# Kernel optimization log

Hardware: AMD Instinct MI355X
Metric: run time of the kernel (lower is better)

## Reference

```python
import jax, jax.numpy as jnp
import numpy as np

N_NODES = 50000
N_EDGES = 800000
DIM_IN = 64
DIM_HID = 128
DIM_OUT = 64


def _linear_init(key, fan_in, fan_out):
    # torch nn.Linear default: U(-1/sqrt(fan_in), 1/sqrt(fan_in)) for W and b
    kw, kb = jax.random.split(key)
    bound = 1.0 / np.sqrt(fan_in)
    W = jax.random.uniform(kw, (fan_in, fan_out), minval=-bound, maxval=bound, dtype=jnp.float32)
    b = jax.random.uniform(kb, (fan_out,), minval=-bound, maxval=bound, dtype=jnp.float32)
    return W, b


def setup_inputs() -> dict:
    key = jax.random.key(0)
    kx, ke, k0, k1, k2 = jax.random.split(key, 5)
    x = jax.random.normal(kx, (N_NODES, DIM_IN), dtype=jnp.float32)
    edge_idx = jax.random.randint(ke, (2, N_EDGES), 0, N_NODES, dtype=jnp.int64)
    W0, b0 = _linear_init(k0, 2 * DIM_IN, DIM_HID)
    W1, b1 = _linear_init(k1, DIM_HID, DIM_HID)
    W2, b2 = _linear_init(k2, DIM_HID, DIM_OUT)
    return {"x": x, "edge_idx": edge_idx, "W0": W0, "b0": b0,
            "W1": W1, "b1": b1, "W2": W2, "b2": b2}


def reference(x, edge_idx, W0, b0, W1, b1, W2, b2):
    row, col = edge_idx[0], edge_idx[1]
    # gather + concat edge features: [E, 2*dim_in]
    h = jnp.concatenate([x[row], x[col]], axis=-1)
    h = jax.nn.softplus(h @ W0 + b0)
    h = jax.nn.softplus(h @ W1 + b1)
    h = h @ W2 + b2  # [E, dim_out]
    # scatter-add edge messages to source nodes
    return jax.ops.segment_sum(h, row, num_segments=x.shape[0])
```

## Files before the change

### kernel.cpp

```cpp
#include <hip/hip_runtime.h>
#include <math.h>

#define N_NODES 50000
#define N_EDGES 800000
#define DIM_IN 64
#define DIM_HID 128
#define DIM_OUT 64
#define PAD 136

typedef __attribute__((ext_vector_type(8))) short short8;
typedef __attribute__((ext_vector_type(4))) float f32x4;

union U8 { uint4 u; short8 s; };

__device__ __forceinline__ unsigned short f2bf(float f) {
    unsigned u = __float_as_uint(f);
    return (unsigned short)((u + 0x7fffu + ((u >> 16) & 1u)) >> 16);
}

__device__ __forceinline__ unsigned cvt_pk_bf16(float a, float b) {
    unsigned d;
    asm("v_cvt_pk_bf16_f32 %0, %1, %2" : "=v"(d) : "v"(a), "v"(b));
    return d;
}

__device__ __forceinline__ float exp2_fast(float a) {
#if __has_builtin(__builtin_amdgcn_exp2f)
    return __builtin_amdgcn_exp2f(a);
#else
    return __expf(a * 0.69314718f);
#endif
}

__device__ __forceinline__ unsigned sp2(float x0, float x1) {
    const float L2E = 1.44269504f;
    float z0 = exp2_fast(-fabsf(x0) * L2E);
    float z1 = exp2_fast(-fabsf(x1) * L2E);
    float p0 = fmaf(fmaf(fmaf(-0.1011458f, z0, 0.2942925f), z0, -0.5f), z0, 1.0f) * z0;
    float p1 = fmaf(fmaf(fmaf(-0.1011458f, z1, 0.2942925f), z1, -0.5f), z1, 1.0f) * z1;
    return cvt_pk_bf16(fmaxf(x0, 0.0f) + p0, fmaxf(x1, 0.0f) + p1);
}

__global__ void prep_all(const float* __restrict__ x,
                         const float* __restrict__ W0,
                         const float* __restrict__ W1,
                         const float* __restrict__ W2,
                         unsigned short* __restrict__ wt,
                         unsigned short* __restrict__ xbf,
                         float4* __restrict__ outz) {
    int i = blockIdx.x * blockDim.x + threadIdx.x;

    if (i < (N_NODES * DIM_OUT / 4))
        outz[i] = make_float4(0.f, 0.f, 0.f, 0.f);

    if (i < (N_NODES * DIM_IN / 4)) {
        float4 v = *((const float4*)x + i);
        uint2 p;
        p.x = cvt_pk_bf16(v.x, v.y);
        p.y = cvt_pk_bf16(v.z, v.w);
        *((uint2*)xbf + i) = p;
    }

    if (i < 320 * PAD) {
        int row = i / PAD, s = i - row * PAD;
        float v = 0.f;
        if (s < 128) {
            int f = ((s >> 5) << 5) | (((s & 7) >> 2) << 4) | (((s >> 3) & 3) << 2) | (s & 3);
            if (row < 128)      v = W0[s * DIM_HID + row];
            else if (row < 256) v = W1[f * DIM_HID + (row - 128)];
            else                v = W2[f * DIM_OUT + (row - 256)];
        }
        wt[i] = f2bf(v);
    }
}

__global__ void prep_weights(const float* __restrict__ W0,
                             const float* __restrict__ W1,
                             const float* __restrict__ W2,
                             unsigned short* __restrict__ wt) {
    int i = blockIdx.x * blockDim.x + threadIdx.x;
    if (i >= 320 * PAD) return;
    int row = i / PAD, s = i - row * PAD;
    float v = 0.f;
    if (s < 128) {
        int f = ((s >> 5) << 5) | (((s & 7) >> 2) << 4) | (((s >> 3) & 3) << 2) | (s & 3);
        if (row < 128)      v = W0[s * DIM_HID + row];
        else if (row < 256) v = W1[f * DIM_HID + (row - 128)];
        else                v = W2[f * DIM_OUT + (row - 256)];
    }
    wt[i] = f2bf(v);
}

template <bool XB>
__global__ __launch_bounds__(256, 4)
void edge_mlp_mfma(const float* __restrict__ x,
                   const unsigned short* __restrict__ xbf,
                   const int* __restrict__ eidx,
                   const unsigned short* __restrict__ wt,
                   const float* __restrict__ b0,
                   const float* __restrict__ b1,
                   const float* __restrict__ b2,
                   float* __restrict__ out) {
    const int lane = threadIdx.x & 63;
    const int w    = threadIdx.x >> 6;
    const int l16  = lane & 15;
    const int q    = lane >> 4;
    const int e0w  = blockIdx.x * 128 + w * 32;

    const unsigned short* Wt0 = wt;
    const unsigned short* Wt1 = wt + 128 * PAD;
    const unsigned short* Wt2 = wt + 256 * PAD;

    int nodeR[2], nodeC[2];
#pragma unroll
    for (int m = 0; m < 2; ++m) {
        nodeR[m] = eidx[e0w + m * 16 + l16];
        nodeC[m] = eidx[N_EDGES + e0w + m * 16 + l16];
    }

    short8 hfr[2][4];
#pragma unroll
    for (int m = 0; m < 2; ++m)
#pragma unroll
        for (int kk = 0; kk < 4; ++kk) {
            int node = (kk >= 2) ? nodeC[m] : nodeR[m];
            if (XB) {
                hfr[m][kk] = *(const short8*)(xbf + (size_t)node * DIM_IN + (kk & 1) * 32 + q * 8);
            } else {
                const float* p = x + (size_t)node * DIM_IN + (kk & 1) * 32 + q * 8;
                float4 v0 = *(const float4*)p;
                float4 v1 = *(const float4*)(p + 4);
                U8 t;
                t.u.x = cvt_pk_bf16(v0.x, v0.y);
                t.u.y = cvt_pk_bf16(v0.z, v0.w);
                t.u.z = cvt_pk_bf16(v1.x, v1.y);
                t.u.w = cvt_pk_bf16(v1.z, v1.w);
                hfr[m][kk] = t.s;
            }
        }

#pragma unroll
    for (int L = 0; L < 2; ++L) {
        const unsigned short* W = L ? Wt1 : Wt0;
        const float* bias = L ? b1 : b0;
        unsigned d[2][8][2];
#pragma unroll
        for (int ti = 0; ti < 8; ++ti) {
            f32x4 bb = *(const f32x4*)(bias + ti * 16 + q * 4);
            f32x4 a0 = bb, a1 = bb;
            const unsigned short* Wp = W + (ti * 16 + l16) * PAD + q * 8;
            short8 wf[4];
#pragma unroll
            for (int kk = 0; kk < 4; ++kk)
                wf[kk] = *(const short8*)(Wp + kk * 32);
#pragma unroll
            for (int kk = 0; kk < 4; ++kk) {
                a0 = __builtin_amdgcn_mfma_f32_16x16x32_bf16(wf[kk], hfr[0][kk], a0, 0, 0, 0);
                a1 = __builtin_amdgcn_mfma_f32_16x16x32_bf16(wf[kk], hfr[1][kk], a1, 0, 0, 0);
            }
            d[0][ti][0] = sp2(a0[0], a0[1]);
            d[0][ti][1] = sp2(a0[2], a0[3]);
            d[1][ti][0] = sp2(a1[0], a1[1]);
            d[1][ti][1] = sp2(a1[2], a1[3]);
        }
#pragma unroll
        for (int m = 0; m < 2; ++m)
#pragma unroll
            for (int kk = 0; kk < 4; ++kk) {
                U8 t;
                t.u.x = d[m][2 * kk][0];
                t.u.y = d[m][2 * kk][1];
                t.u.z = d[m][2 * kk + 1][0];
                t.u.w = d[m][2 * kk + 1][1];
                hfr[m][kk] = t.s;
            }
    }

    int nodeO[2][4];
#pragma unroll
    for (int m = 0; m < 2; ++m)
#pragma unroll
        for (int r = 0; r < 4; ++r)
            nodeO[m][r] = eidx[e0w + m * 16 + q * 4 + r];

#pragma unroll
    for (int ti = 0; ti < 4; ++ti) {
        float bv = b2[ti * 16 + l16];
        f32x4 a0 = (f32x4){bv, bv, bv, bv};
        f32x4 a1 = a0;
        const unsigned short* Wp = Wt2 + (ti * 16 + l16) * PAD + q * 8;
        short8 wf[4];
#pragma unroll
        for (int kk = 0; kk < 4; ++kk)
            wf[kk] = *(const short8*)(Wp + kk * 32);
#pragma unroll
        for (int kk = 0; kk < 4; ++kk) {
            a0 = __builtin_amdgcn_mfma_f32_16x16x32_bf16(hfr[0][kk], wf[kk], a0, 0, 0, 0);
            a1 = __builtin_amdgcn_mfma_f32_16x16x32_bf16(hfr[1][kk], wf[kk], a1, 0, 0, 0);
        }
#pragma unroll
        for (int r = 0; r < 4; ++r) {
            atomicAdd(out + (size_t)nodeO[0][r] * DIM_OUT + ti * 16 + l16, a0[r]);
            atomicAdd(out + (size_t)nodeO[1][r] * DIM_OUT + ti * 16 + l16, a1[r]);
        }
    }
}

extern "C" void kernel_launch(void* const* d_in, const int* in_sizes, int n_in,
                              void* d_out, int out_size, void* d_ws, size_t ws_size,
                              hipStream_t stream) {
    const float* x  = (const float*)d_in[0];
    const int*   ei = (const int*)d_in[1];
    const float* W0 = (const float*)d_in[2];
    const float* b0 = (const float*)d_in[3];
    const float* W1 = (const float*)d_in[4];
    const float* b1 = (const float*)d_in[5];
    const float* W2 = (const float*)d_in[6];
    const float* b2 = (const float*)d_in[7];
    float* out = (float*)d_out;

    unsigned short* wt = (unsigned short*)d_ws;
    const size_t WT_BYTES = (size_t)320 * PAD * sizeof(unsigned short);
    unsigned short* xbf = (unsigned short*)((char*)d_ws + WT_BYTES);
    const size_t need = WT_BYTES + (size_t)N_NODES * DIM_IN * sizeof(unsigned short);

    if (ws_size >= need) {
        prep_all<<<(N_NODES * DIM_IN / 4 + 255) / 256, 256, 0, stream>>>(
            x, W0, W1, W2, wt, xbf, (float4*)out);
        edge_mlp_mfma<true><<<N_EDGES / 128, 256, 0, stream>>>(
            x, xbf, ei, wt, b0, b1, b2, out);
    } else {
        hipMemsetAsync(out, 0, (size_t)N_NODES * DIM_OUT * sizeof(float), stream);
        const int wn = 320 * PAD;
        prep_weights<<<(wn + 255) / 256, 256, 0, stream>>>(W0, W1, W2, wt);
        edge_mlp_mfma<false><<<N_EDGES / 128, 256, 0, stream>>>(
            x, nullptr, ei, wt, b0, b1, b2, out);
    }
}
```

Measured before the change: 274.8 us.

## Counting-sort edges by source node and pre-reduce messages before atomics

Adds a counting sort of edges by row: a histogram kernel, a single-block scan and an atomic scatter that writes sorted row and column arrays. The MLP kernel then reads edges in sorted order. Each lane sums the consecutive outputs that share a destination node before issuing float atomics, cutting atomic traffic and contention and improving gather locality. The cost is three extra launches plus the scatter atomics. The fallback path now passes wt as the xbf pointer to prep_all, so the x conversion can overwrite the packed weights there.

```diff
diff --git a/kernel.cpp b/kernel.cpp
--- a/kernel.cpp
+++ b/kernel.cpp
@@ -47,7 +47,8 @@
                          const float* __restrict__ W2,
                          unsigned short* __restrict__ wt,
                          unsigned short* __restrict__ xbf,
-                         float4* __restrict__ outz) {
+                         float4* __restrict__ outz,
+                         int* __restrict__ hist) {
     int i = blockIdx.x * blockDim.x + threadIdx.x;
 
     if (i < (N_NODES * DIM_OUT / 4))
@@ -60,6 +61,8 @@
         p.y = cvt_pk_bf16(v.z, v.w);
         *((uint2*)xbf + i) = p;
     }
+
+    if (hist && i < N_NODES) hist[i] = 0;
 
     if (i < 320 * PAD) {
         int row = i / PAD, s = i - row * PAD;
@@ -74,27 +77,56 @@
     }
 }
 
-__global__ void prep_weights(const float* __restrict__ W0,
-                             const float* __restrict__ W1,
-                             const float* __restrict__ W2,
-                             unsigned short* __restrict__ wt) {
+__global__ void hist_kernel(const int* __restrict__ eidx, int* __restrict__ hist) {
     int i = blockIdx.x * blockDim.x + threadIdx.x;
-    if (i >= 320 * PAD) return;
-    int row = i / PAD, s = i - row * PAD;
-    float v = 0.f;
-    if (s < 128) {
-        int f = ((s >> 5) << 5) | (((s & 7) >> 2) << 4) | (((s >> 3) & 3) << 2) | (s & 3);
-        if (row < 128)      v = W0[s * DIM_HID + row];
-        else if (row < 256) v = W1[f * DIM_HID + (row - 128)];
-        else                v = W2[f * DIM_OUT + (row - 256)];
-    }
-    wt[i] = f2bf(v);
-}
-
-template <bool XB>
+    if (i < N_EDGES) atomicAdd(&hist[eidx[i]], 1);
+}
+
+__global__ __launch_bounds__(1024)
+void scan_bins(const int* __restrict__ hist, int* __restrict__ cursor) {
+    __shared__ int part[1024];
+    const int t = threadIdx.x;
+    const int CH = (N_NODES + 1023) / 1024;
+    const int base = t * CH;
+    int s = 0;
+    for (int j = 0; j < CH; ++j) {
+        int b = base + j;
+        if (b < N_NODES) s += hist[b];
+    }
+    part[t] = s;
+    __syncthreads();
+    for (int off = 1; off < 1024; off <<= 1) {
+        int u = (t >= off) ? part[t - off] : 0;
+        __syncthreads();
+        part[t] += u;
+        __syncthreads();
+    }
+    int run = (t == 0) ? 0 : part[t - 1];
+    for (int j = 0; j < CH; ++j) {
+        int b = base + j;
+        if (b < N_NODES) { cursor[b] = run; run += hist[b]; }
+    }
+}
+
+__global__ void scatter_kernel(const int* __restrict__ eidx,
+                               int* __restrict__ cursor,
+                               int* __restrict__ srow,
+                               int* __restrict__ scol) {
+    int i = blockIdx.x * blockDim.x + threadIdx.x;
+    if (i >= N_EDGES) return;
+    int r = eidx[i];
+    int c = eidx[N_EDGES + i];
+    int pos = atomicAdd(&cursor[r], 1);
+    srow[pos] = r;
+    scol[pos] = c;
+}
+
+template <int MODE>
 __global__ __launch_bounds__(256, 4)
 void edge_mlp_mfma(const float* __restrict__ x,
                    const unsigned short* __restrict__ xbf,
+                   const int* __restrict__ srow,
+                   const int* __restrict__ scol,
                    const int* __restrict__ eidx,
                    const unsigned short* __restrict__ wt,
                    const float* __restrict__ b0,
@@ -114,9 +146,22 @@
     int nodeR[2], nodeC[2];
 #pragma unroll
     for (int m = 0; m < 2; ++m) {
-        nodeR[m] = eidx[e0w + m * 16 + l16];
-        nodeC[m] = eidx[N_EDGES + e0w + m * 16 + l16];
-    }
+        if (MODE == 2) {
+            nodeR[m] = srow[e0w + m * 16 + l16];
+            nodeC[m] = scol[e0w + m * 16 + l16];
+        } else {
+            nodeR[m] = eidx[e0w + m * 16 + l16];
+            nodeC[m] = eidx[N_EDGES + e0w + m * 16 + l16];
+        }
+    }
+
+    int ns[8];
+#pragma unroll
+    for (int m = 0; m < 2; ++m)
+#pragma unroll
+        for (int r = 0; r < 4; ++r)
+            ns[m * 4 + r] = (MODE == 2) ? srow[e0w + m * 16 + q * 4 + r]
+                                        : eidx[e0w + m * 16 + q * 4 + r];
 
     short8 hfr[2][4];
 #pragma unroll
@@ -124,7 +169,7 @@
 #pragma unroll
         for (int kk = 0; kk < 4; ++kk) {
             int node = (kk >= 2) ? nodeC[m] : nodeR[m];
-            if (XB) {
+            if (MODE >= 1) {
                 hfr[m][kk] = *(const short8*)(xbf + (size_t)node * DIM_IN + (kk & 1) * 32 + q * 8);
             } else {
                 const float* p = x + (size_t)node * DIM_IN + (kk & 1) * 32 + q * 8;
@@ -176,32 +221,60 @@
             }
     }
 
-    int nodeO[2][4];
-#pragma unroll
-    for (int m = 0; m < 2; ++m)
-#pragma unroll
-        for (int r = 0; r < 4; ++r)
-            nodeO[m][r] = eidx[e0w + m * 16 + q * 4 + r];
-
-#pragma unroll
-    for (int ti = 0; ti < 4; ++ti) {
-        float bv = b2[ti * 16 + l16];
-        f32x4 a0 = (f32x4){bv, bv, bv, bv};
-        f32x4 a1 = a0;
-        const unsigned short* Wp = Wt2 + (ti * 16 + l16) * PAD + q * 8;
-        short8 wf[4];
-#pragma unroll
-        for (int kk = 0; kk < 4; ++kk)
-            wf[kk] = *(const short8*)(Wp + kk * 32);
-#pragma unroll
-        for (int kk = 0; kk < 4; ++kk) {
-            a0 = __builtin_amdgcn_mfma_f32_16x16x32_bf16(hfr[0][kk], wf[kk], a0, 0, 0, 0);
-            a1 = __builtin_amdgcn_mfma_f32_16x16x32_bf16(hfr[1][kk], wf[kk], a1, 0, 0, 0);
-        }
-#pragma unroll
-        for (int r = 0; r < 4; ++r) {
-            atomicAdd(out + (size_t)nodeO[0][r] * DIM_OUT + ti * 16 + l16, a0[r]);
-            atomicAdd(out + (size_t)nodeO[1][r] * DIM_OUT + ti * 16 + l16, a1[r]);
+    {
+        f32x4 acc[4][2];
+#pragma unroll
+        for (int ti = 0; ti < 4; ++ti) {
+            float bv = b2[ti * 16 + l16];
+            f32x4 a0 = (f32x4){bv, bv, bv, bv};
+            f32x4 a1 = a0;
+            const unsigned short* Wp = Wt2 + (ti * 16 + l16) * PAD + q * 8;
+            short8 wf[4];
+#pragma unroll
+            for (int kk = 0; kk < 4; ++kk)
+                wf[kk] = *(const short8*)(Wp + kk * 32);
+#pragma unroll
+            for (int kk = 0; kk < 4; ++kk) {
+                a0 = __builtin_amdgcn_mfma_f32_16x16x32_bf16(hfr[0][kk], wf[kk], a0, 0, 0, 0);
+                a1 = __builtin_amdgcn_mfma_f32_16x16x32_bf16(hfr[1][kk], wf[kk], a1, 0, 0, 0);
+            }
+            acc[ti][0] = a0;
+            acc[ti][1] = a1;
+        }
+
+        if (MODE == 2) {
+            int curn = ns[0];
+            float c0 = 0.f, c1 = 0.f, c2 = 0.f, c3 = 0.f;
+#pragma unroll
+            for (int s = 0; s < 8; ++s) {
+                const int m = s >> 2, r = s & 3;
+                if (s > 0 && ns[s] != curn) {
+                    float* o = out + (size_t)curn * DIM_OUT + l16;
+                    atomicAdd(o +  0, c0);
+                    atomicAdd(o + 16, c1);
+                    atomicAdd(o + 32, c2);
+                    atomicAdd(o + 48, c3);
+                    c0 = c1 = c2 = c3 = 0.f;
+                    curn = ns[s];
+                }
+                c0 += acc[0][m][r];
+                c1 += acc[1][m][r];
+                c2 += acc[2][m][r];
+                c3 += acc[3][m][r];
+            }
+            float* o = out + (size_t)curn * DIM_OUT + l16;
+            atomicAdd(o +  0, c0);
+            atomicAdd(o + 16, c1);
+            atomicAdd(o + 32, c2);
+            atomicAdd(o + 48, c3);
+        } else {
+#pragma unroll
+            for (int ti = 0; ti < 4; ++ti)
+#pragma unroll
+                for (int r = 0; r < 4; ++r) {
+                    atomicAdd(out + (size_t)ns[r] * DIM_OUT + ti * 16 + l16, acc[ti][0][r]);
+                    atomicAdd(out + (size_t)ns[4 + r] * DIM_OUT + ti * 16 + l16, acc[ti][1][r]);
+                }
         }
     }
 }
@@ -219,21 +292,40 @@
     const float* b2 = (const float*)d_in[7];
     float* out = (float*)d_out;
 
-    unsigned short* wt = (unsigned short*)d_ws;
-    const size_t WT_BYTES = (size_t)320 * PAD * sizeof(unsigned short);
-    unsigned short* xbf = (unsigned short*)((char*)d_ws + WT_BYTES);
-    const size_t need = WT_BYTES + (size_t)N_NODES * DIM_IN * sizeof(unsigned short);
-
-    if (ws_size >= need) {
+    char* ws = (char*)d_ws;
+    const size_t WT_BYTES   = (size_t)320 * PAD * 2;
+    const size_t XBF_BYTES  = (size_t)N_NODES * DIM_IN * 2;
+    const size_t HIST_BYTES = 200192;
+    const size_t SROW_BYTES = (size_t)N_EDGES * 4;
+
+    unsigned short* wt  = (unsigned short*)ws;
+    unsigned short* xbf = (unsigned short*)(ws + WT_BYTES);
+    int* hist   = (int*)(ws + WT_BYTES + XBF_BYTES);
+    int* cursor = (int*)(ws + WT_BYTES + XBF_BYTES + HIST_BYTES);
+    int* srow   = (int*)(ws + WT_BYTES + XBF_BYTES + 2 * HIST_BYTES);
+    int* scol   = (int*)(ws + WT_BYTES + XBF_BYTES + 2 * HIST_BYTES + SROW_BYTES);
+
+    const size_t need_sorted = WT_BYTES + XBF_BYTES + 2 * HIST_BYTES + 2 * SROW_BYTES;
+    const size_t need_xbf    = WT_BYTES + XBF_BYTES;
+
+    if (ws_size >= need_sorted) {
         prep_all<<<(N_NODES * DIM_IN / 4 + 255) / 256, 256, 0, stream>>>(
-            x, W0, W1, W2, wt, xbf, (float4*)out);
-        edge_mlp_mfma<true><<<N_EDGES / 128, 256, 0, stream>>>(
-            x, xbf, ei, wt, b0, b1, b2, out);
+            x, W0, W1, W2, wt, xbf, (float4*)out, hist);
+        hist_kernel<<<(N_EDGES + 255) / 256, 256, 0, stream>>>(ei, hist);
+        scan_bins<<<1, 1024, 0, stream>>>(hist, cursor);
+        scatter_kernel<<<(N_EDGES + 255) / 256, 256, 0, stream>>>(ei, cursor, srow, scol);
+        edge_mlp_mfma<2><<<N_EDGES / 128, 256, 0, stream>>>(
+            x, xbf, srow, scol, ei, wt, b0, b1, b2, out);
+    } else if (ws_size >= need_xbf) {
+        prep_all<<<(N_NODES * DIM_IN / 4 + 255) / 256, 256, 0, stream>>>(
+            x, W0, W1, W2, wt, xbf, (float4*)out, nullptr);
+        edge_mlp_mfma<1><<<N_EDGES / 128, 256, 0, stream>>>(
+            x, xbf, nullptr, nullptr, ei, wt, b0, b1, b2, out);
     } else {
         hipMemsetAsync(out, 0, (size_t)N_NODES * DIM_OUT * sizeof(float), stream);
-        const int wn = 320 * PAD;
-        prep_weights<<<(wn + 255) / 256, 256, 0, stream>>>(W0, W1, W2, wt);
-        edge_mlp_mfma<false><<<N_EDGES / 128, 256, 0, stream>>>(
-            x, nullptr, ei, wt, b0, b1, b2, out);
-    }
-}
+        prep_all<<<(N_NODES * DIM_IN / 4 + 255) / 256, 256, 0, stream>>>(
+            x, W0, W1, W2, wt, (unsigned short*)wt, (float4*)out, nullptr);
+        edge_mlp_mfma<0><<<N_EDGES / 128, 256, 0, stream>>>(
+            x, nullptr, nullptr, nullptr, ei, wt, b0, b1, b2, out);
+    }
+}
```

Result: slower. 448.6 us (+63.3%).

## Stage layer weights in LDS per block instead of global loads

Applied to the files above, without the earlier changes.

Each block copies the bf16 weight matrix for the current layer into a 34 KB shared buffer and reads MFMA operand fragments from LDS rather than global/L2. The buffer is reloaded between layers, with barriers around each copy, and the destination-node index loads are moved earlier. The final-layer results are gathered into registers before the atomic scatter. This trades repeated global weight reads for per-block copy traffic, extra syncs and LDS that may limit occupancy.

```diff
diff --git a/kernel.cpp b/kernel.cpp
--- a/kernel.cpp
+++ b/kernel.cpp
@@ -101,22 +101,27 @@
                    const float* __restrict__ b1,
                    const float* __restrict__ b2,
                    float* __restrict__ out) {
+    __shared__ unsigned short lw[128 * PAD];
+
     const int lane = threadIdx.x & 63;
     const int w    = threadIdx.x >> 6;
     const int l16  = lane & 15;
     const int q    = lane >> 4;
     const int e0w  = blockIdx.x * 128 + w * 32;
 
-    const unsigned short* Wt0 = wt;
-    const unsigned short* Wt1 = wt + 128 * PAD;
-    const unsigned short* Wt2 = wt + 256 * PAD;
-
     int nodeR[2], nodeC[2];
 #pragma unroll
     for (int m = 0; m < 2; ++m) {
         nodeR[m] = eidx[e0w + m * 16 + l16];
         nodeC[m] = eidx[N_EDGES + e0w + m * 16 + l16];
     }
+
+    int ns[8];
+#pragma unroll
+    for (int m = 0; m < 2; ++m)
+#pragma unroll
+        for (int r = 0; r < 4; ++r)
+            ns[m * 4 + r] = eidx[e0w + m * 16 + q * 4 + r];
 
     short8 hfr[2][4];
 #pragma unroll
@@ -139,16 +144,22 @@
             }
         }
 
+    {
+        const uint4* src = (const uint4*)wt;
+        uint4* dst = (uint4*)lw;
+        for (int i = threadIdx.x; i < 2176; i += 256) dst[i] = src[i];
+    }
+    __syncthreads();
+
 #pragma unroll
     for (int L = 0; L < 2; ++L) {
-        const unsigned short* W = L ? Wt1 : Wt0;
         const float* bias = L ? b1 : b0;
         unsigned d[2][8][2];
 #pragma unroll
         for (int ti = 0; ti < 8; ++ti) {
             f32x4 bb = *(const f32x4*)(bias + ti * 16 + q * 4);
             f32x4 a0 = bb, a1 = bb;
-            const unsigned short* Wp = W + (ti * 16 + l16) * PAD + q * 8;
+            const unsigned short* Wp = lw + (ti * 16 + l16) * PAD + q * 8;
             short8 wf[4];
 #pragma unroll
             for (int kk = 0; kk < 4; ++kk)
@@ -174,35 +185,44 @@
                 t.u.w = d[m][2 * kk + 1][1];
                 hfr[m][kk] = t.s;
             }
-    }
-
-    int nodeO[2][4];
-#pragma unroll
-    for (int m = 0; m < 2; ++m)
-#pragma unroll
-        for (int r = 0; r < 4; ++r)
-            nodeO[m][r] = eidx[e0w + m * 16 + q * 4 + r];
-
-#pragma unroll
-    for (int ti = 0; ti < 4; ++ti) {
-        float bv = b2[ti * 16 + l16];
-        f32x4 a0 = (f32x4){bv, bv, bv, bv};
-        f32x4 a1 = a0;
-        const unsigned short* Wp = Wt2 + (ti * 16 + l16) * PAD + q * 8;
-        short8 wf[4];
-#pragma unroll
-        for (int kk = 0; kk < 4; ++kk)
-            wf[kk] = *(const short8*)(Wp + kk * 32);
-#pragma unroll
-        for (int kk = 0; kk < 4; ++kk) {
-            a0 = __builtin_amdgcn_mfma_f32_16x16x32_bf16(hfr[0][kk], wf[kk], a0, 0, 0, 0);
-            a1 = __builtin_amdgcn_mfma_f32_16x16x32_bf16(hfr[1][kk], wf[kk], a1, 0, 0, 0);
-        }
-#pragma unroll
-        for (int r = 0; r < 4; ++r) {
-            atomicAdd(out + (size_t)nodeO[0][r] * DIM_OUT + ti * 16 + l16, a0[r]);
-            atomicAdd(out + (size_t)nodeO[1][r] * DIM_OUT + ti * 16 + l16, a1[r]);
-        }
+        __syncthreads();
+        {
+            const uint4* src = (const uint4*)(wt + (size_t)(L ? 256 : 128) * PAD);
+            uint4* dst = (uint4*)lw;
+            const int n = L ? 1088 : 2176;
+            for (int i = threadIdx.x; i < n; i += 256) dst[i] = src[i];
+        }
+        __syncthreads();
+    }
+
+    {
+        f32x4 acc[4][2];
+#pragma unroll
+        for (int ti = 0; ti < 4; ++ti) {
+            float bv = b2[ti * 16 + l16];
+            f32x4 a0 = (f32x4){bv, bv, bv, bv};
+            f32x4 a1 = a0;
+            const unsigned short* Wp = lw + (ti * 16 + l16) * PAD + q * 8;
+            short8 wf[4];
+#pragma unroll
+            for (int kk = 0; kk < 4; ++kk)
+                wf[kk] = *(const short8*)(Wp + kk * 32);
+#pragma unroll
+            for (int kk = 0; kk < 4; ++kk) {
+                a0 = __builtin_amdgcn_mfma_f32_16x16x32_bf16(hfr[0][kk], wf[kk], a0, 0, 0, 0);
+                a1 = __builtin_amdgcn_mfma_f32_16x16x32_bf16(hfr[1][kk], wf[kk], a1, 0, 0, 0);
+            }
+            acc[ti][0] = a0;
+            acc[ti][1] = a1;
+        }
+
+#pragma unroll
+        for (int ti = 0; ti < 4; ++ti)
+#pragma unroll
+            for (int r = 0; r < 4; ++r) {
+                atomicAdd(out + (size_t)ns[r] * DIM_OUT + ti * 16 + l16, acc[ti][0][r]);
+                atomicAdd(out + (size_t)ns[4 + r] * DIM_OUT + ti * 16 + l16, acc[ti][1][r]);
+            }
     }
 }
 
@@ -231,8 +251,7 @@
             x, xbf, ei, wt, b0, b1, b2, out);
     } else {
         hipMemsetAsync(out, 0, (size_t)N_NODES * DIM_OUT * sizeof(float), stream);
-        const int wn = 320 * PAD;
-        prep_weights<<<(wn + 255) / 256, 256, 0, stream>>>(W0, W1, W2, wt);
+        prep_weights<<<(320 * PAD + 255) / 256, 256, 0, stream>>>(W0, W1, W2, wt);
         edge_mlp_mfma<false><<<N_EDGES / 128, 256, 0, stream>>>(
             x, nullptr, ei, wt, b0, b1, b2, out);
     }
```

Result: faster. 266.7 us (-2.9%).
